# Kernel tuning notes

Hardware: AMD Instinct MI355X
Metric: run time of the kernel (lower is better)

## Reference

```python
import jax, jax.numpy as jnp
import numpy as np

CLASSES = 80
CELLS = 7
SEG = CLASSES + 5        # per-cell segment: [x, y, w, h, conf, class_scores...]
NCELLS = CELLS ** 2
BATCH = 16384


def setup_inputs() -> dict:
    key = jax.random.key(0)
    x = jax.random.normal(key, (BATCH, NCELLS * SEG), dtype=jnp.float32)
    return {"input_": x}


def reference(input_):
    B = input_.shape[0]
    x = input_.reshape(B, NCELLS, SEG)
    # Original loop only processes the first NCELLS-1 cells (off-by-one kept faithfully).
    act = x[:, : NCELLS - 1, :]                      # [B, 48, SEG]
    box_xy = jax.nn.sigmoid(act[..., 0:2])           # sigmoid on x,y
    wh = act[..., 2:4]                               # untouched
    conf = jax.nn.sigmoid(act[..., 4:5])             # sigmoid on confidence
    cls = jax.nn.softmax(act[..., 5:], axis=-1)      # softmax over class scores
    act_out = jnp.concatenate([box_xy, wh, conf, cls], axis=-1)
    out = jnp.concatenate([act_out, x[:, NCELLS - 1 :, :]], axis=1)
    return out.reshape(B, NCELLS * SEG)
```

## Files before the change

### kernel.cpp

```cpp
#include <hip/hip_runtime.h>
#include <hip/hip_bf16.h>
#include <math.h>


#define SEG 85
#define NCELLS 49

__global__ __launch_bounds__(256) void yolo_act_kernel(
    const float* __restrict__ in, float* __restrict__ out, int nseg) {
  const int wave = (int)((blockIdx.x * (unsigned)blockDim.x + threadIdx.x) >> 6);
  const int lane = threadIdx.x & 63;
  if (wave >= nseg) return;

  const int cell = wave % NCELLS;
  const long long base = (long long)wave * SEG;

  const float v0 = in[base + lane];
  const bool has2 = (lane + 64) < SEG;
  const float v1 = has2 ? in[base + 64 + lane] : 0.0f;

  if (cell == NCELLS - 1) {
    out[base + lane] = v0;
    if (has2) out[base + 64 + lane] = v1;
    return;
  }

  float m = (lane >= 5) ? v0 : -INFINITY;
  if (has2) m = fmaxf(m, v1);
  #pragma unroll
  for (int off = 32; off >= 1; off >>= 1)
    m = fmaxf(m, __shfl_xor(m, off, 64));

  const float e0 = (lane >= 5) ? __expf(v0 - m) : 0.0f;
  const float e1 = has2 ? __expf(v1 - m) : 0.0f;
  float s = e0 + e1;
  #pragma unroll
  for (int off = 32; off >= 1; off >>= 1)
    s += __shfl_xor(s, off, 64);
  const float inv = 1.0f / s;

  float r0;
  if (lane < 2)       r0 = 1.0f / (1.0f + __expf(-v0));
  else if (lane < 4)  r0 = v0;
  else if (lane == 4) r0 = 1.0f / (1.0f + __expf(-v0));
  else                r0 = e0 * inv;

  out[base + lane] = r0;
  if (has2) out[base + 64 + lane] = e1 * inv;
}

extern "C" void kernel_launch(void* const* d_in, const int* in_sizes, int n_in,
                              void* d_out, int out_size, void* d_ws, size_t ws_size,
                              hipStream_t stream) {
  const float* in = (const float*)d_in[0];
  float* out = (float*)d_out;
  const int nseg = in_sizes[0] / SEG;
  const int waves_per_block = 256 / 64;
  const int grid = (nseg + waves_per_block - 1) / waves_per_block;
  yolo_act_kernel<<<grid, 256, 0, stream>>>(in, out, nseg);
}
```

Baseline: 524.2 us.

## Stage segments through LDS with float4 copies and thread-per-segment softmax

```diff
diff --git a/kernel.cpp b/kernel.cpp
--- a/kernel.cpp
+++ b/kernel.cpp
@@ -5,48 +5,79 @@
 
 #define SEG 85
 #define NCELLS 49
+#define TPB 128
+#define WORDS_PER_BLK (TPB * SEG)
+#define F4_PER_BLK (WORDS_PER_BLK / 4)
 
-__global__ __launch_bounds__(256) void yolo_act_kernel(
-    const float* __restrict__ in, float* __restrict__ out, int nseg) {
-  const int wave = (int)((blockIdx.x * (unsigned)blockDim.x + threadIdx.x) >> 6);
-  const int lane = threadIdx.x & 63;
-  if (wave >= nseg) return;
+__global__ __launch_bounds__(TPB) void yolo_act_kernel(
+    const float* __restrict__ in, float* __restrict__ out) {
+  __shared__ __align__(16) float lds[WORDS_PER_BLK];
+  __shared__ float inv_s[TPB + 1];
 
-  const int cell = wave % NCELLS;
-  const long long base = (long long)wave * SEG;
+  const int tid = threadIdx.x;
+  const long long blk_word = (long long)blockIdx.x * WORDS_PER_BLK;
 
-  const float v0 = in[base + lane];
-  const bool has2 = (lane + 64) < SEG;
-  const float v1 = has2 ? in[base + 64 + lane] : 0.0f;
+  {
+    const float4* __restrict__ gsrc = (const float4*)(in + blk_word);
+    float4* ldst = (float4*)lds;
+    #pragma unroll
+    for (int it = 0; it < F4_PER_BLK / TPB; ++it)
+      ldst[tid + it * TPB] = gsrc[tid + it * TPB];
+    const int rem = F4_PER_BLK - (F4_PER_BLK / TPB) * TPB;
+    if (tid < rem)
+      ldst[tid + (F4_PER_BLK / TPB) * TPB] = gsrc[tid + (F4_PER_BLK / TPB) * TPB];
+  }
+  __syncthreads();
 
-  if (cell == NCELLS - 1) {
-    out[base + lane] = v0;
-    if (has2) out[base + 64 + lane] = v1;
-    return;
+  {
+    const int seg_global = blockIdx.x * TPB + tid;
+    const int cell = seg_global % NCELLS;
+    float* p = lds + tid * SEG;
+    if (cell != NCELLS - 1) {
+      float s0 = 0.f, s1 = 0.f, s2 = 0.f, s3 = 0.f;
+      #pragma unroll
+      for (int i = 5; i < SEG; i += 4) {
+        float e0 = __expf(p[i + 0]);
+        float e1 = __expf(p[i + 1]);
+        float e2 = __expf(p[i + 2]);
+        float e3 = __expf(p[i + 3]);
+        p[i + 0] = e0; p[i + 1] = e1; p[i + 2] = e2; p[i + 3] = e3;
+        s0 += e0; s1 += e1; s2 += e2; s3 += e3;
+      }
+      p[0] = 1.f / (1.f + __expf(-p[0]));
+      p[1] = 1.f / (1.f + __expf(-p[1]));
+      p[4] = 1.f / (1.f + __expf(-p[4]));
+      inv_s[tid] = 1.f / ((s0 + s1) + (s2 + s3));
+    } else {
+      inv_s[tid] = -1.f;
+    }
+    if (tid == 0) inv_s[TPB] = -1.f;
   }
+  __syncthreads();
 
-  float m = (lane >= 5) ? v0 : -INFINITY;
-  if (has2) m = fmaxf(m, v1);
-  #pragma unroll
-  for (int off = 32; off >= 1; off >>= 1)
-    m = fmaxf(m, __shfl_xor(m, off, 64));
-
-  const float e0 = (lane >= 5) ? __expf(v0 - m) : 0.0f;
-  const float e1 = has2 ? __expf(v1 - m) : 0.0f;
-  float s = e0 + e1;
-  #pragma unroll
-  for (int off = 32; off >= 1; off >>= 1)
-    s += __shfl_xor(s, off, 64);
-  const float inv = 1.0f / s;
-
-  float r0;
-  if (lane < 2)       r0 = 1.0f / (1.0f + __expf(-v0));
-  else if (lane < 4)  r0 = v0;
-  else if (lane == 4) r0 = 1.0f / (1.0f + __expf(-v0));
-  else                r0 = e0 * inv;
-
-  out[base + lane] = r0;
-  if (has2) out[base + 64 + lane] = e1 * inv;
+  {
+    float4* __restrict__ gdst = (float4*)(out + blk_word);
+    const float4* lsrc = (const float4*)lds;
+    for (int k = tid; k < F4_PER_BLK; k += TPB) {
+      float4 v = lsrc[k];
+      const int w = k * 4;
+      const int seg0 = w / SEG;
+      const int off0 = w - seg0 * SEG;
+      const float sc0 = inv_s[seg0];
+      const float sc1 = inv_s[seg0 + 1];
+      float r[4] = {v.x, v.y, v.z, v.w};
+      #pragma unroll
+      for (int j = 0; j < 4; ++j) {
+        const int o = off0 + j;
+        const bool cross = (o >= SEG);
+        const float sc = cross ? sc1 : sc0;
+        const int off = cross ? (o - SEG) : o;
+        if (off >= 5 && sc > 0.f) r[j] *= sc;
+      }
+      v.x = r[0]; v.y = r[1]; v.z = r[2]; v.w = r[3];
+      gdst[k] = v;
+    }
+  }
 }
 
 extern "C" void kernel_launch(void* const* d_in, const int* in_sizes, int n_in,
@@ -55,7 +86,6 @@
   const float* in = (const float*)d_in[0];
   float* out = (float*)d_out;
   const int nseg = in_sizes[0] / SEG;
-  const int waves_per_block = 256 / 64;
-  const int grid = (nseg + waves_per_block - 1) / waves_per_block;
-  yolo_act_kernel<<<grid, 256, 0, stream>>>(in, out, nseg);
+  const int grid = nseg / TPB;
+  yolo_act_kernel<<<grid, TPB, 0, stream>>>(in, out);
 }
```

Result: faster. 442.4 us (-15.6%).
